# Optimization experiments

Hardware: AMD Instinct MI355X
Metric: run time of the kernel (lower is better)

Reference implementation:

```python
import jax, jax.numpy as jnp
import numpy as np

ALPHA = 0.5
GAMMA = 2.0
NUM_CLASSES = 80


def calc_iou(a, b):
    # a: [A,4] anchors, b: [M,4] gt boxes (x1,y1,x2,y2) -> IoU [A,M]
    area_b = (b[:, 2] - b[:, 0]) * (b[:, 3] - b[:, 1])
    area_a = (a[:, 2] - a[:, 0]) * (a[:, 3] - a[:, 1])
    iw = jnp.minimum(a[:, None, 2], b[None, :, 2]) - jnp.maximum(a[:, None, 0], b[None, :, 0])
    ih = jnp.minimum(a[:, None, 3], b[None, :, 3]) - jnp.maximum(a[:, None, 1], b[None, :, 1])
    iw = jnp.maximum(iw, 0.0)
    ih = jnp.maximum(ih, 0.0)
    inter = iw * ih
    ua = jnp.maximum(area_a[:, None] + area_b[None, :] - inter, 1e-8)
    return inter / ua


def _per_image(cls, reg, ann, anchor):
    # cls: [A,C], reg: [A,4], ann: [M,5], anchor: [A,4]
    C = cls.shape[-1]
    c = jnp.clip(cls, 1e-4, 1.0 - 1e-4)

    aw = anchor[:, 2] - anchor[:, 0]
    ah = anchor[:, 3] - anchor[:, 1]
    acx = anchor[:, 0] + 0.5 * aw
    acy = anchor[:, 1] + 0.5 * ah

    iou = calc_iou(anchor, ann[:, :4])          # [A,M]
    iou_max = jnp.max(iou, axis=1)               # [A]
    iou_arg = jnp.argmax(iou, axis=1)            # [A]
    assigned = ann[iou_arg]                      # [A,5]

    pos = iou_max >= 0.5                         # [A]
    labels = assigned[:, 4].astype(jnp.int32)
    onehot = (labels[:, None] == jnp.arange(C)[None, :]).astype(c.dtype)
    # targets: 1 for assigned class on positives, 0 elsewhere on positives,
    # 0 for clear negatives (IoU<0.4), -1 (ignore) in between.
    targets = jnp.where(pos[:, None], onehot,
                        jnp.where((iou_max < 0.4)[:, None], 0.0, -1.0))

    is_one = targets == 1.0
    alpha_factor = jnp.where(is_one, ALPHA, 1.0 - ALPHA)
    focal_weight = jnp.where(is_one, 1.0 - c, c)
    focal_weight = alpha_factor * focal_weight ** GAMMA
    bce = -(targets * jnp.log(c) + (1.0 - targets) * jnp.log(1.0 - c))
    cls_loss = jnp.where(targets != -1.0, focal_weight * bce, 0.0)

    num_pos = jnp.sum(pos)
    cls_out = cls_loss.sum() / jnp.maximum(num_pos.astype(c.dtype), 1.0)

    gw = assigned[:, 2] - assigned[:, 0]
    gh = assigned[:, 3] - assigned[:, 1]
    gcx = assigned[:, 0] + 0.5 * gw
    gcy = assigned[:, 1] + 0.5 * gh
    gw = jnp.maximum(gw, 1.0)
    gh = jnp.maximum(gh, 1.0)
    tdx = (gcx - acx) / aw
    tdy = (gcy - acy) / ah
    tdw = jnp.log(gw / aw)
    tdh = jnp.log(gh / ah)
    t = jnp.stack([tdx, tdy, tdw, tdh], axis=1) / jnp.array([0.1, 0.1, 0.2, 0.2], dtype=c.dtype)

    diff = jnp.abs(t - reg)
    smooth_l1 = jnp.where(diff <= 1.0 / 9.0, 0.5 * 9.0 * diff ** 2, diff - 0.5 / 9.0)
    smooth_l1 = jnp.where(pos[:, None], smooth_l1, 0.0)
    denom = jnp.maximum(num_pos.astype(c.dtype) * 4.0, 1.0)
    reg_out = jnp.where(num_pos > 0, smooth_l1.sum() / denom, 0.0)
    return cls_out, reg_out


def setup_inputs() -> dict:
    key = jax.random.key(0)
    B, A, C, M = 8, 65536, NUM_CLASSES, 32
    k1, k2, k3, k4, k5, k6, k7 = jax.random.split(key, 7)
    classifications = jax.random.uniform(k1, (B, A, C), dtype=jnp.float32)
    regressions = jax.random.normal(k2, (B, A, 4), dtype=jnp.float32)
    # anchors: valid boxes from centers + sizes over a 512x512 image
    actr = jax.random.uniform(k3, (A, 2), minval=0.0, maxval=512.0)
    asz = jax.random.uniform(k4, (A, 2), minval=16.0, maxval=256.0)
    anchors = jnp.concatenate([actr - 0.5 * asz, actr + 0.5 * asz], axis=1)[None].astype(jnp.float32)
    # annotations: valid gt boxes with class labels in [0, C)
    gctr = jax.random.uniform(k5, (B, M, 2), minval=32.0, maxval=480.0)
    gsz = jax.random.uniform(k6, (B, M, 2), minval=16.0, maxval=256.0)
    boxes = jnp.concatenate([gctr - 0.5 * gsz, gctr + 0.5 * gsz], axis=2)
    labels = jax.random.randint(k7, (B, M, 1), 0, C).astype(jnp.float32)
    annotations = jnp.concatenate([boxes, labels], axis=2).astype(jnp.float32)
    return {"classifications": classifications, "regressions": regressions,
            "anchors": anchors, "annotations": annotations}


def reference(classifications, regressions, anchors, annotations):
    anchor = anchors[0]
    cls_l, reg_l = jax.vmap(_per_image, in_axes=(0, 0, 0, None))(
        classifications, regressions, annotations, anchor)
    return (jnp.mean(cls_l, keepdims=True), jnp.mean(reg_l, keepdims=True))
```

## Files before the change

### kernel.cpp

```cpp
#include <hip/hip_runtime.h>
#include <math.h>


static constexpr int   kC     = 80;
static constexpr int   kTA    = 256;
static constexpr int   kBlock = 256;
static constexpr int   kMaxM  = 32;

__global__ void init_ws_kernel(double* acc, int* pos, int B) {
    int t = threadIdx.x;
    if (t < B) { acc[t] = 0.0; acc[B + t] = 0.0; pos[t] = 0; }
}

__device__ __forceinline__ float elem_loss(float c, int k, int f) {
    c = fminf(fmaxf(c, 1e-4f), 1.0f - 1e-4f);
    bool one = (k == f);
    float w = one ? (1.0f - c) : c;
    float l = one ? c : (1.0f - c);
    return 0.5f * w * w * (-__logf(l));
}

__global__ __launch_bounds__(kBlock) void focal_main(
        const float* __restrict__ cls,
        const float* __restrict__ reg,
        const float* __restrict__ anc,
        const float* __restrict__ ann,
        double* __restrict__ cls_sum,
        double* __restrict__ reg_sum,
        int*    __restrict__ pos_cnt,
        int A, int M)
{
    const int b  = blockIdx.y;
    const int a0 = blockIdx.x * kTA;
    const int t  = threadIdx.x;

    __shared__ float s_box[kMaxM][6];
    __shared__ int   s_flag[kTA];

    if (t < M) {
        const float* p = ann + ((size_t)b * M + t) * 5;
        float x1 = p[0], y1 = p[1], x2 = p[2], y2 = p[3], lb = p[4];
        s_box[t][0] = x1; s_box[t][1] = y1;
        s_box[t][2] = x2; s_box[t][3] = y2;
        s_box[t][4] = (x2 - x1) * (y2 - y1);
        s_box[t][5] = lb;
    }
    __syncthreads();

    const int a = a0 + t;
    const float4 ab = *reinterpret_cast<const float4*>(anc + (size_t)a * 4);
    const float aw = ab.z - ab.x;
    const float ah = ab.w - ab.y;
    const float area_a = aw * ah;

    float best = -1.0f;
    int bestj = 0;
    #pragma unroll 8
    for (int j = 0; j < M; ++j) {
        float iw = fminf(ab.z, s_box[j][2]) - fmaxf(ab.x, s_box[j][0]);
        float ih = fminf(ab.w, s_box[j][3]) - fmaxf(ab.y, s_box[j][1]);
        iw = fmaxf(iw, 0.0f);
        ih = fmaxf(ih, 0.0f);
        float inter = iw * ih;
        float ua = fmaxf(area_a + s_box[j][4] - inter, 1e-8f);
        float iou = inter / ua;
        if (iou > best) { best = iou; bestj = j; }
    }
    const bool pos = (best >= 0.5f);
    const int flag = pos ? (int)s_box[bestj][5] : ((best < 0.4f) ? -2 : -1);
    s_flag[t] = flag;

    float regLoss = 0.0f;
    int   posInt  = pos ? 1 : 0;
    if (pos) {
        float gx1 = s_box[bestj][0], gy1 = s_box[bestj][1];
        float gx2 = s_box[bestj][2], gy2 = s_box[bestj][3];
        float gw = gx2 - gx1, gh = gy2 - gy1;
        float gcx = gx1 + 0.5f * gw, gcy = gy1 + 0.5f * gh;
        gw = fmaxf(gw, 1.0f);
        gh = fmaxf(gh, 1.0f);
        float acx = ab.x + 0.5f * aw, acy = ab.y + 0.5f * ah;
        float t0 = ((gcx - acx) / aw) / 0.1f;
        float t1 = ((gcy - acy) / ah) / 0.1f;
        float t2 = logf(gw / aw) / 0.2f;
        float t3 = logf(gh / ah) / 0.2f;
        const float4 rg = *reinterpret_cast<const float4*>(reg + ((size_t)b * A + a) * 4);
        float d0 = fabsf(t0 - rg.x), d1 = fabsf(t1 - rg.y);
        float d2 = fabsf(t2 - rg.z), d3 = fabsf(t3 - rg.w);
        const float th = 1.0f / 9.0f, csh = 0.5f / 9.0f;
        regLoss  = (d0 <= th) ? 4.5f * d0 * d0 : d0 - csh;
        regLoss += (d1 <= th) ? 4.5f * d1 * d1 : d1 - csh;
        regLoss += (d2 <= th) ? 4.5f * d2 * d2 : d2 - csh;
        regLoss += (d3 <= th) ? 4.5f * d3 * d3 : d3 - csh;
    }
    __syncthreads();

    const float4* cbase =
        reinterpret_cast<const float4*>(cls + ((size_t)b * A + a0) * kC);
    constexpr int F4A  = kC / 4;
    constexpr int ITER = kTA * F4A / kBlock;
    float clsLoss = 0.0f;
    #pragma unroll 4
    for (int i = 0; i < ITER; ++i) {
        int idx = i * kBlock + t;
        int al  = idx / F4A;
        int kb  = (idx - al * F4A) * 4;
        int f   = s_flag[al];
        float4 v = cbase[idx];
        if (f != -1) {
            clsLoss += elem_loss(v.x, kb + 0, f);
            clsLoss += elem_loss(v.y, kb + 1, f);
            clsLoss += elem_loss(v.z, kb + 2, f);
            clsLoss += elem_loss(v.w, kb + 3, f);
        }
    }

    #pragma unroll
    for (int off = 32; off > 0; off >>= 1) {
        clsLoss += __shfl_down(clsLoss, off);
        regLoss += __shfl_down(regLoss, off);
        posInt  += __shfl_down(posInt,  off);
    }
    __shared__ float s_cls[kBlock / 64];
    __shared__ float s_reg[kBlock / 64];
    __shared__ int   s_pos[kBlock / 64];
    const int wid = t >> 6, lane = t & 63;
    if (lane == 0) { s_cls[wid] = clsLoss; s_reg[wid] = regLoss; s_pos[wid] = posInt; }
    __syncthreads();
    if (t == 0) {
        float cs = 0.0f, rs = 0.0f; int ps = 0;
        #pragma unroll
        for (int w = 0; w < kBlock / 64; ++w) { cs += s_cls[w]; rs += s_reg[w]; ps += s_pos[w]; }
        atomicAdd(&cls_sum[b], (double)cs);
        atomicAdd(&reg_sum[b], (double)rs);
        atomicAdd(&pos_cnt[b], ps);
    }
}

__global__ void finalize_kernel(const double* __restrict__ cls_sum,
                                const double* __restrict__ reg_sum,
                                const int* __restrict__ pos_cnt,
                                float* __restrict__ out, int B)
{
    if (threadIdx.x == 0 && blockIdx.x == 0) {
        double co = 0.0, ro = 0.0;
        for (int b = 0; b < B; ++b) {
            double np = (double)pos_cnt[b];
            co += cls_sum[b] / fmax(np, 1.0);
            ro += (pos_cnt[b] > 0) ? reg_sum[b] / (np * 4.0) : 0.0;
        }
        out[0] = (float)(co / B);
        out[1] = (float)(ro / B);
    }
}

extern "C" void kernel_launch(void* const* d_in, const int* in_sizes, int n_in,
                              void* d_out, int out_size, void* d_ws, size_t ws_size,
                              hipStream_t stream)
{
    const float* cls = (const float*)d_in[0];
    const float* reg = (const float*)d_in[1];
    const float* anc = (const float*)d_in[2];
    const float* ann = (const float*)d_in[3];

    const int A = in_sizes[2] / 4;
    const int B = in_sizes[1] / (A * 4);
    const int M = in_sizes[3] / (B * 5);

    double* acc = (double*)d_ws;
    int*    pos = (int*)(acc + 2 * B);
    float*  out = (float*)d_out;

    hipLaunchKernelGGL(init_ws_kernel, dim3(1), dim3(64), 0, stream, acc, pos, B);

    dim3 grid(A / kTA, B);
    hipLaunchKernelGGL(focal_main, grid, dim3(kBlock), 0, stream,
                       cls, reg, anc, ann, acc, acc + B, pos, A, M);

    hipLaunchKernelGGL(finalize_kernel, dim3(1), dim3(1), 0, stream,
                       acc, acc + B, pos, out, B);
}
```

Baseline: 255.8 us.

## Replace double atomics with per-block partials and parallel finalize; nontemporal loads

Each block now writes its partial cls/reg/pos sums to its own slot in the workspace instead of doing double-precision atomicAdds into per-image accumulators. This removes the init kernel launch and atomic contention. The finalize kernel becomes a one-wave-per-image parallel reduction over the partials. Streaming loads of classifications and regressions use nontemporal hints to avoid polluting cache. The finalize launch uses 64*B threads, so it depends on B being at most 16 per the shared arrays.

```diff
diff --git a/kernel.cpp b/kernel.cpp
--- a/kernel.cpp
+++ b/kernel.cpp
@@ -1,16 +1,14 @@
 #include <hip/hip_runtime.h>
 #include <math.h>
 
+
+typedef float f32x4 __attribute__((ext_vector_type(4)));
 
 static constexpr int   kC     = 80;
 static constexpr int   kTA    = 256;
 static constexpr int   kBlock = 256;
 static constexpr int   kMaxM  = 32;
-
-__global__ void init_ws_kernel(double* acc, int* pos, int B) {
-    int t = threadIdx.x;
-    if (t < B) { acc[t] = 0.0; acc[B + t] = 0.0; pos[t] = 0; }
-}
+static constexpr int   kMaxB  = 16;
 
 __device__ __forceinline__ float elem_loss(float c, int k, int f) {
     c = fminf(fmaxf(c, 1e-4f), 1.0f - 1e-4f);
@@ -25,9 +23,9 @@
         const float* __restrict__ reg,
         const float* __restrict__ anc,
         const float* __restrict__ ann,
-        double* __restrict__ cls_sum,
-        double* __restrict__ reg_sum,
-        int*    __restrict__ pos_cnt,
+        float* __restrict__ clsPart,
+        float* __restrict__ regPart,
+        int*   __restrict__ posPart,
         int A, int M)
 {
     const int b  = blockIdx.y;
@@ -48,7 +46,7 @@
     __syncthreads();
 
     const int a = a0 + t;
-    const float4 ab = *reinterpret_cast<const float4*>(anc + (size_t)a * 4);
+    const f32x4 ab = *reinterpret_cast<const f32x4*>(anc + (size_t)a * 4);
     const float aw = ab.z - ab.x;
     const float ah = ab.w - ab.y;
     const float area_a = aw * ah;
@@ -84,7 +82,8 @@
         float t1 = ((gcy - acy) / ah) / 0.1f;
         float t2 = logf(gw / aw) / 0.2f;
         float t3 = logf(gh / ah) / 0.2f;
-        const float4 rg = *reinterpret_cast<const float4*>(reg + ((size_t)b * A + a) * 4);
+        const f32x4 rg = __builtin_nontemporal_load(
+            reinterpret_cast<const f32x4*>(reg + ((size_t)b * A + a) * 4));
         float d0 = fabsf(t0 - rg.x), d1 = fabsf(t1 - rg.y);
         float d2 = fabsf(t2 - rg.z), d3 = fabsf(t3 - rg.w);
         const float th = 1.0f / 9.0f, csh = 0.5f / 9.0f;
@@ -95,8 +94,8 @@
     }
     __syncthreads();
 
-    const float4* cbase =
-        reinterpret_cast<const float4*>(cls + ((size_t)b * A + a0) * kC);
+    const f32x4* cbase =
+        reinterpret_cast<const f32x4*>(cls + ((size_t)b * A + a0) * kC);
     constexpr int F4A  = kC / 4;
     constexpr int ITER = kTA * F4A / kBlock;
     float clsLoss = 0.0f;
@@ -106,7 +105,7 @@
         int al  = idx / F4A;
         int kb  = (idx - al * F4A) * 4;
         int f   = s_flag[al];
-        float4 v = cbase[idx];
+        f32x4 v = __builtin_nontemporal_load(&cbase[idx]);
         if (f != -1) {
             clsLoss += elem_loss(v.x, kb + 0, f);
             clsLoss += elem_loss(v.y, kb + 1, f);
@@ -131,23 +130,45 @@
         float cs = 0.0f, rs = 0.0f; int ps = 0;
         #pragma unroll
         for (int w = 0; w < kBlock / 64; ++w) { cs += s_cls[w]; rs += s_reg[w]; ps += s_pos[w]; }
-        atomicAdd(&cls_sum[b], (double)cs);
-        atomicAdd(&reg_sum[b], (double)rs);
-        atomicAdd(&pos_cnt[b], ps);
-    }
-}
-
-__global__ void finalize_kernel(const double* __restrict__ cls_sum,
-                                const double* __restrict__ reg_sum,
-                                const int* __restrict__ pos_cnt,
-                                float* __restrict__ out, int B)
+        const int part = b * gridDim.x + blockIdx.x;
+        clsPart[part] = cs;
+        regPart[part] = rs;
+        posPart[part] = ps;
+    }
+}
+
+__global__ void finalize_kernel(const float* __restrict__ clsPart,
+                                const float* __restrict__ regPart,
+                                const int*   __restrict__ posPart,
+                                float* __restrict__ out,
+                                int nPerImg, int B)
 {
-    if (threadIdx.x == 0 && blockIdx.x == 0) {
+    const int w = threadIdx.x >> 6;
+    const int l = threadIdx.x & 63;
+    float cs = 0.0f, rs = 0.0f; int ps = 0;
+    if (w < B) {
+        for (int i = l; i < nPerImg; i += 64) {
+            int idx = w * nPerImg + i;
+            cs += clsPart[idx]; rs += regPart[idx]; ps += posPart[idx];
+        }
+    }
+    #pragma unroll
+    for (int off = 32; off > 0; off >>= 1) {
+        cs += __shfl_down(cs, off);
+        rs += __shfl_down(rs, off);
+        ps += __shfl_down(ps, off);
+    }
+    __shared__ double s_c[kMaxB];
+    __shared__ double s_r[kMaxB];
+    __shared__ int    s_p[kMaxB];
+    if (l == 0 && w < B) { s_c[w] = cs; s_r[w] = rs; s_p[w] = ps; }
+    __syncthreads();
+    if (threadIdx.x == 0) {
         double co = 0.0, ro = 0.0;
         for (int b = 0; b < B; ++b) {
-            double np = (double)pos_cnt[b];
-            co += cls_sum[b] / fmax(np, 1.0);
-            ro += (pos_cnt[b] > 0) ? reg_sum[b] / (np * 4.0) : 0.0;
+            double np = (double)s_p[b];
+            co += s_c[b] / fmax(np, 1.0);
+            ro += (s_p[b] > 0) ? s_r[b] / (np * 4.0) : 0.0;
         }
         out[0] = (float)(co / B);
         out[1] = (float)(ro / B);
@@ -167,16 +188,18 @@
     const int B = in_sizes[1] / (A * 4);
     const int M = in_sizes[3] / (B * 5);
 
-    double* acc = (double*)d_ws;
-    int*    pos = (int*)(acc + 2 * B);
-    float*  out = (float*)d_out;
-
-    hipLaunchKernelGGL(init_ws_kernel, dim3(1), dim3(64), 0, stream, acc, pos, B);
-
-    dim3 grid(A / kTA, B);
+    const int nBlkX = A / kTA;
+    const int nPart = B * nBlkX;
+
+    float* clsPart = (float*)d_ws;
+    float* regPart = clsPart + nPart;
+    int*   posPart = (int*)(regPart + nPart);
+    float* out     = (float*)d_out;
+
+    dim3 grid(nBlkX, B);
     hipLaunchKernelGGL(focal_main, grid, dim3(kBlock), 0, stream,
-                       cls, reg, anc, ann, acc, acc + B, pos, A, M);
-
-    hipLaunchKernelGGL(finalize_kernel, dim3(1), dim3(1), 0, stream,
-                       acc, acc + B, pos, out, B);
-}
+                       cls, reg, anc, ann, clsPart, regPart, posPart, A, M);
+
+    hipLaunchKernelGGL(finalize_kernel, dim3(1), dim3(64 * B), 0, stream,
+                       clsPart, regPart, posPart, out, nBlkX, B);
+}
```

After: 248.2 us. 2.9% less time.
